# Performance work log

Measured on AMD Instinct MI355X. Metric: run time of the kernel, lower is better.

Reference implementation:

```python
import jax, jax.numpy as jnp
import numpy as np

C_IN, C_OUT, K, PAD, STRIDE = 128, 256, 3, 1, 1
H = W = 256


def setup_inputs() -> dict:
    key = jax.random.key(0)
    k1, k2, k3 = jax.random.split(key, 3)
    # batch=1: the original forward uses X_pad[0] for every batch index,
    # so with m=1 the buggy loop and a standard conv are mathematically identical.
    x = jax.random.normal(k1, (1, C_IN, H, W), dtype=jnp.float32)
    # nn.Parameter(torch.rand(...)) -> uniform[0,1)
    weight = jax.random.uniform(k2, (C_OUT, C_IN, K, K), dtype=jnp.float32)
    bias = jax.random.uniform(k3, (C_OUT,), dtype=jnp.float32)
    return {"x": x, "weight": weight, "bias": bias}


def reference(x, weight, bias):
    # Faithful math of convAppx.forward with FP_appx_mul treated as exact
    # multiply (FP_appx_mul is not defined in the source): a plain 2D
    # cross-correlation (no kernel flip, matching the sliced elementwise
    # product) with symmetric padding, stride 1, plus per-channel bias.
    z = jax.lax.conv_general_dilated(
        x, weight,
        window_strides=(STRIDE, STRIDE),
        padding=((PAD, PAD), (PAD, PAD)),
        dimension_numbers=("NCHW", "OIHW", "NCHW"),
    )
    return z + bias[None, :, None, None]
```

## Files before the change

kernel.cpp:

```cpp
#include <hip/hip_runtime.h>
#include <hip/hip_bf16.h>


typedef short bf16x8 __attribute__((ext_vector_type(8)));
typedef float f32x4 __attribute__((ext_vector_type(4)));
typedef unsigned short u16x4 __attribute__((ext_vector_type(4)));
typedef unsigned short u16x8 __attribute__((ext_vector_type(8)));

#define CIN   128
#define COUT  256
#define HH    256
#define WW    256
#define HP    258
#define ROWP  (HP * CIN)

static __device__ __forceinline__ unsigned short f2bf(float v) {
    __hip_bfloat16 b = __float2bfloat16(v);
    return *reinterpret_cast<unsigned short*>(&b);
}

static __device__ __forceinline__ void gload_lds16(const unsigned short* g, unsigned short* l) {
    __builtin_amdgcn_global_load_lds(
        (const __attribute__((address_space(1))) unsigned int*)g,
        (__attribute__((address_space(3))) unsigned int*)l, 16, 0, 0);
}

__global__ __launch_bounds__(256) void prep_kernel(const float* __restrict__ x,
                                                   const float* __restrict__ w,
                                                   unsigned short* __restrict__ xb,
                                                   unsigned short* __restrict__ wr) {
    int bid = blockIdx.x;
    int t   = threadIdx.x;

    if (bid < 65) {
        int i = bid * 256 + t;
        if (i < 16448) {
            u16x8 z = {0, 0, 0, 0, 0, 0, 0, 0};
            int off;
            if (i < 8256) {
                int r   = (i >= 4128) ? 1 : 0;
                int rem = i - r * 4128;
                off = (r * 257) * ROWP + rem * 8;
            } else {
                int j   = i - 8256;
                int col = j >> 12;
                int rem = j & 4095;
                int hp  = (rem >> 4) + 1;
                int c8  = rem & 15;
                off = hp * ROWP + (col * 257) * CIN + c8 * 8;
            }
            *(u16x8*)(&xb[off]) = z;
        }
    }

    if (bid < 128) {
        int p = bid * 256 + t;
        const float* src = w + p * 9;
        #pragma unroll
        for (int khw = 0; khw < 9; ++khw)
            wr[khw * (COUT * CIN) + p] = f2bf(src[khw]);
    }

    int h  = bid >> 2;
    int w0 = (bid & 3) * 64;
    __shared__ unsigned short tile[CIN * 72];

    int wq  = t & 15;
    int cib = t >> 4;
    for (int c0 = 0; c0 < CIN; c0 += 16) {
        int ci = c0 + cib;
        float4 v = *(const float4*)(x + ci * (HH * WW) + h * WW + w0 + wq * 4);
        u16x4 p;
        p.x = f2bf(v.x); p.y = f2bf(v.y); p.z = f2bf(v.z); p.w = f2bf(v.w);
        *(u16x4*)(&tile[ci * 72 + wq * 4]) = p;
    }
    __syncthreads();

    for (int it = 0; it < 4; ++it) {
        int idx = it * 256 + t;
        int ww_ = idx & 63;
        int c8  = idx >> 6;
        u16x8 o;
        #pragma unroll
        for (int j = 0; j < 8; ++j)
            o[j] = tile[(c8 * 8 + j) * 72 + ww_];
        int dst = ((h + 1) * HP + (w0 + ww_ + 1)) * CIN + c8 * 8;
        *(u16x8*)(&xb[dst]) = o;
    }
}

__global__ __launch_bounds__(512, 2) void conv_mfma_kernel(const unsigned short* __restrict__ xb,
                                                           const unsigned short* __restrict__ wr,
                                                           const float* __restrict__ bias,
                                                           float* __restrict__ out) {
    __shared__ unsigned short Bw[258 * 128];
    __shared__ unsigned short Ah[2][256 * 64];

    int bid = blockIdx.x;
    int h   = (bid & 7) * 32 + (bid >> 3);

    int t    = threadIdx.x;
    int lane = t & 63;
    int wave = t >> 6;
    int wm   = wave >> 1;
    int wn   = wave & 1;
    int quad = lane >> 4;
    int l16  = lane & 15;

    f32x4 acc[4][8];
    #pragma unroll
    for (int mi = 0; mi < 4; ++mi)
        #pragma unroll
        for (int ni = 0; ni < 8; ++ni)
            acc[mi][ni] = (f32x4){0.f, 0.f, 0.f, 0.f};

    auto stageA = [&](int idx, unsigned short* dst) {
        int khw_  = idx >> 1;
        int half_ = idx & 1;
        const unsigned short* wsrc = wr + (size_t)khw_ * (COUT * CIN) + half_ * 64;
        #pragma unroll
        for (int it = 0; it < 4; ++it) {
            int seg = it * 512 + t;
            int r   = seg >> 3;
            int s   = seg & 7;
            int c   = s ^ (r & 7);
            gload_lds16(wsrc + r * CIN + c * 8, &dst[seg * 8]);
        }
    };

    stageA(0, Ah[0]);

    for (int i = 0; i < 18; ++i) {
        int khw  = i >> 1;
        int half = i & 1;
        int kw   = khw % 3;

        if ((i % 6) == 0) {
            const unsigned short* xrow = xb + (size_t)(h + i / 6) * ROWP;
            #pragma unroll
            for (int it = 0; it < 8; ++it) {
                int seg = it * 512 + t;
                int col = seg >> 4;
                int s   = seg & 15;
                int c   = s ^ (col & 15);
                gload_lds16(xrow + col * CIN + c * 8, &Bw[seg * 8]);
            }
            if (t < 32) {
                int seg = 4096 + t;
                int col = seg >> 4;
                int s   = seg & 15;
                int c   = s ^ (col & 15);
                gload_lds16(xrow + col * CIN + c * 8, &Bw[seg * 8]);
            }
        }

        int nxt = (i + 1) % 18;
        stageA(nxt, Ah[nxt & 1]);

        asm volatile("s_waitcnt vmcnt(4)" ::: "memory");
        __builtin_amdgcn_s_barrier();
        __builtin_amdgcn_sched_barrier(0);

        const unsigned short* Acur = Ah[i & 1];
        __builtin_amdgcn_s_setprio(1);
        #pragma unroll
        for (int kkk = 0; kkk < 2; ++kkk) {
            int lc = kkk * 4 + quad;
            int cg = half * 8 + lc;
            bf16x8 af[4], bfr[8];
            #pragma unroll
            for (int mi = 0; mi < 4; ++mi) {
                int row = wm * 64 + mi * 16 + l16;
                af[mi] = *(bf16x8*)(&Acur[row * 64 + (lc ^ (l16 & 7)) * 8]);
            }
            #pragma unroll
            for (int ni = 0; ni < 8; ++ni) {
                int col = wn * 128 + ni * 16 + l16 + kw;
                bfr[ni] = *(bf16x8*)(&Bw[col * 128 + (cg ^ (col & 15)) * 8]);
            }
            #pragma unroll
            for (int mi = 0; mi < 4; ++mi)
                #pragma unroll
                for (int ni = 0; ni < 8; ++ni)
                    acc[mi][ni] = __builtin_amdgcn_mfma_f32_16x16x32_bf16(
                        af[mi], bfr[ni], acc[mi][ni], 0, 0, 0);
        }
        __builtin_amdgcn_s_setprio(0);

        asm volatile("s_waitcnt lgkmcnt(0)" ::: "memory");
        __builtin_amdgcn_s_barrier();
        __builtin_amdgcn_sched_barrier(0);
    }

    int sp0 = wn * 128 + l16;
    #pragma unroll
    for (int mi = 0; mi < 4; ++mi) {
        #pragma unroll
        for (int r = 0; r < 4; ++r) {
            int co = wm * 64 + mi * 16 + quad * 4 + r;
            float b = bias[co];
            float* orow = out + (size_t)co * (HH * WW) + h * WW + sp0;
            #pragma unroll
            for (int ni = 0; ni < 8; ++ni)
                orow[ni * 16] = acc[mi][ni][r] + b;
        }
    }
}

extern "C" void kernel_launch(void* const* d_in, const int* in_sizes, int n_in,
                              void* d_out, int out_size, void* d_ws, size_t ws_size,
                              hipStream_t stream) {
    const float* x    = (const float*)d_in[0];
    const float* w    = (const float*)d_in[1];
    const float* bias = (const float*)d_in[2];
    float* out        = (float*)d_out;

    unsigned short* xb = (unsigned short*)d_ws;
    unsigned short* wr = xb + (size_t)HP * HP * CIN;

    prep_kernel<<<dim3(1024), dim3(256), 0, stream>>>(x, w, xb, wr);
    conv_mfma_kernel<<<dim3(256), dim3(512), 0, stream>>>(xb, wr, bias, out);
}
```

Before: 136.2 us.

## Split input row into channel halves and interleave MFMA phases with barriers

The single full-channel input-row LDS buffer is replaced by two 64-channel half buffers, so the next input row can be prefetched one half at a time instead of reloading all 128 channels at once. The weight double buffer is now indexed by channel half. Each half-step is split into four phases: fragment reads, then an MFMA burst, with workgroup barriers around them. This ping-pong style schedule aims to overlap LDS reads with matrix math across waves and to hide global-to-LDS loads. The halo columns of the input tile are zeroed in LDS once rather than loaded. The cost is many more barriers per step and a full vmcnt(0) drain at the end of every half-step, which could stall the pipeline.

```diff
diff --git a/kernel.cpp b/kernel.cpp
--- a/kernel.cpp
+++ b/kernel.cpp
@@ -93,7 +93,7 @@
                                                            const unsigned short* __restrict__ wr,
                                                            const float* __restrict__ bias,
                                                            float* __restrict__ out) {
-    __shared__ unsigned short Bw[258 * 128];
+    __shared__ unsigned short Bh[2][258 * 64];
     __shared__ unsigned short Ah[2][256 * 64];
 
     int bid = blockIdx.x;
@@ -114,10 +114,9 @@
         for (int ni = 0; ni < 8; ++ni)
             acc[mi][ni] = (f32x4){0.f, 0.f, 0.f, 0.f};
 
-    auto stageA = [&](int idx, unsigned short* dst) {
-        int khw_  = idx >> 1;
-        int half_ = idx & 1;
+    auto stageA = [&](int khw_, int half_) {
         const unsigned short* wsrc = wr + (size_t)khw_ * (COUT * CIN) + half_ * 64;
+        unsigned short* dst = Ah[half_];
         #pragma unroll
         for (int it = 0; it < 4; ++it) {
             int seg = it * 512 + t;
@@ -127,69 +126,137 @@
             gload_lds16(wsrc + r * CIN + c * 8, &dst[seg * 8]);
         }
     };
-
-    stageA(0, Ah[0]);
-
-    for (int i = 0; i < 18; ++i) {
-        int khw  = i >> 1;
-        int half = i & 1;
-        int kw   = khw % 3;
-
-        if ((i % 6) == 0) {
-            const unsigned short* xrow = xb + (size_t)(h + i / 6) * ROWP;
+    auto stageB = [&](int kh_, int p) {
+        const unsigned short* xrow = xb + (size_t)(h + kh_) * ROWP + p * 64;
+        unsigned short* dst = Bh[p];
+        #pragma unroll
+        for (int it = 0; it < 4; ++it) {
+            int seg = it * 512 + t;
+            int col = (seg >> 3) + 1;
+            int s   = seg & 7;
+            int c   = s ^ (col & 7);
+            gload_lds16(xrow + col * CIN + c * 8, &dst[col * 64 + s * 8]);
+        }
+    };
+
+    if (t < 32) {
+        int buf = t >> 4, colsel = (t >> 3) & 1, s = t & 7;
+        int col = colsel ? 257 : 0;
+        u16x8 z = {0, 0, 0, 0, 0, 0, 0, 0};
+        *(u16x8*)(&Bh[buf][col * 64 + s * 8]) = z;
+    }
+    stageB(0, 0);
+    stageB(0, 1);
+    stageA(0, 0);
+    asm volatile("s_waitcnt vmcnt(0) lgkmcnt(0)" ::: "memory");
+    __builtin_amdgcn_s_barrier();
+    __builtin_amdgcn_sched_barrier(0);
+
+    #pragma unroll 1
+    for (int kh = 0; kh < 3; ++kh) {
+        #pragma unroll
+        for (int kw = 0; kw < 3; ++kw) {
+            int khw = kh * 3 + kw;
             #pragma unroll
-            for (int it = 0; it < 8; ++it) {
-                int seg = it * 512 + t;
-                int col = seg >> 4;
-                int s   = seg & 15;
-                int c   = s ^ (col & 15);
-                gload_lds16(xrow + col * CIN + c * 8, &Bw[seg * 8]);
+            for (int half = 0; half < 2; ++half) {
+                const unsigned short* Acur = Bh[0];
+                Acur = Ah[half];
+                const unsigned short* Bcur = Bh[half];
+                int a_sw = l16 & 7;
+
+                bf16x8 bfr[8], af0, af1, af2, af3;
+
+                {
+                    int lc = quad;
+                    #pragma unroll
+                    for (int ni = 0; ni < 8; ++ni) {
+                        int col = wn * 128 + ni * 16 + l16 + kw;
+                        bfr[ni] = *(bf16x8*)(&Bcur[col * 64 + (lc ^ (col & 7)) * 8]);
+                    }
+                    af0 = *(bf16x8*)(&Acur[(wm * 64 +  0 + l16) * 64 + (lc ^ a_sw) * 8]);
+                    af1 = *(bf16x8*)(&Acur[(wm * 64 + 16 + l16) * 64 + (lc ^ a_sw) * 8]);
+                }
+                if (half == 0) {
+                    if (kw == 0 && kh > 0) stageB(kh, 1);
+                    stageA(khw, 1);
+                } else {
+                    if (kw == 2 && kh < 2) stageB(kh + 1, 0);
+                    stageA((khw == 8) ? 0 : khw + 1, 0);
+                }
+                __builtin_amdgcn_s_barrier();
+                asm volatile("s_waitcnt lgkmcnt(0)" ::: "memory");
+                __builtin_amdgcn_sched_barrier(0);
+                __builtin_amdgcn_s_setprio(1);
+                #pragma unroll
+                for (int ni = 0; ni < 8; ++ni) {
+                    acc[0][ni] = __builtin_amdgcn_mfma_f32_16x16x32_bf16(af0, bfr[ni], acc[0][ni], 0, 0, 0);
+                    acc[1][ni] = __builtin_amdgcn_mfma_f32_16x16x32_bf16(af1, bfr[ni], acc[1][ni], 0, 0, 0);
+                }
+                __builtin_amdgcn_s_setprio(0);
+                __builtin_amdgcn_s_barrier();
+                __builtin_amdgcn_sched_barrier(0);
+
+                {
+                    int lc = quad;
+                    af2 = *(bf16x8*)(&Acur[(wm * 64 + 32 + l16) * 64 + (lc ^ a_sw) * 8]);
+                    af3 = *(bf16x8*)(&Acur[(wm * 64 + 48 + l16) * 64 + (lc ^ a_sw) * 8]);
+                }
+                __builtin_amdgcn_s_barrier();
+                asm volatile("s_waitcnt lgkmcnt(0)" ::: "memory");
+                __builtin_amdgcn_sched_barrier(0);
+                __builtin_amdgcn_s_setprio(1);
+                #pragma unroll
+                for (int ni = 0; ni < 8; ++ni) {
+                    acc[2][ni] = __builtin_amdgcn_mfma_f32_16x16x32_bf16(af2, bfr[ni], acc[2][ni], 0, 0, 0);
+                    acc[3][ni] = __builtin_amdgcn_mfma_f32_16x16x32_bf16(af3, bfr[ni], acc[3][ni], 0, 0, 0);
+                }
+                __builtin_amdgcn_s_setprio(0);
+                __builtin_amdgcn_s_barrier();
+                __builtin_amdgcn_sched_barrier(0);
+
+                {
+                    int lc = 4 + quad;
+                    #pragma unroll
+                    for (int ni = 0; ni < 8; ++ni) {
+                        int col = wn * 128 + ni * 16 + l16 + kw;
+                        bfr[ni] = *(bf16x8*)(&Bcur[col * 64 + (lc ^ (col & 7)) * 8]);
+                    }
+                    af0 = *(bf16x8*)(&Acur[(wm * 64 +  0 + l16) * 64 + (lc ^ a_sw) * 8]);
+                    af1 = *(bf16x8*)(&Acur[(wm * 64 + 16 + l16) * 64 + (lc ^ a_sw) * 8]);
+                }
+                __builtin_amdgcn_s_barrier();
+                asm volatile("s_waitcnt lgkmcnt(0)" ::: "memory");
+                __builtin_amdgcn_sched_barrier(0);
+                __builtin_amdgcn_s_setprio(1);
+                #pragma unroll
+                for (int ni = 0; ni < 8; ++ni) {
+                    acc[0][ni] = __builtin_amdgcn_mfma_f32_16x16x32_bf16(af0, bfr[ni], acc[0][ni], 0, 0, 0);
+                    acc[1][ni] = __builtin_amdgcn_mfma_f32_16x16x32_bf16(af1, bfr[ni], acc[1][ni], 0, 0, 0);
+                }
+                __builtin_amdgcn_s_setprio(0);
+                __builtin_amdgcn_s_barrier();
+                __builtin_amdgcn_sched_barrier(0);
+
+                {
+                    int lc = 4 + quad;
+                    af2 = *(bf16x8*)(&Acur[(wm * 64 + 32 + l16) * 64 + (lc ^ a_sw) * 8]);
+                    af3 = *(bf16x8*)(&Acur[(wm * 64 + 48 + l16) * 64 + (lc ^ a_sw) * 8]);
+                }
+                __builtin_amdgcn_s_barrier();
+                asm volatile("s_waitcnt lgkmcnt(0)" ::: "memory");
+                __builtin_amdgcn_sched_barrier(0);
+                __builtin_amdgcn_s_setprio(1);
+                #pragma unroll
+                for (int ni = 0; ni < 8; ++ni) {
+                    acc[2][ni] = __builtin_amdgcn_mfma_f32_16x16x32_bf16(af2, bfr[ni], acc[2][ni], 0, 0, 0);
+                    acc[3][ni] = __builtin_amdgcn_mfma_f32_16x16x32_bf16(af3, bfr[ni], acc[3][ni], 0, 0, 0);
+                }
+                __builtin_amdgcn_s_setprio(0);
+                asm volatile("s_waitcnt vmcnt(0)" ::: "memory");
+                __builtin_amdgcn_s_barrier();
+                __builtin_amdgcn_sched_barrier(0);
             }
-            if (t < 32) {
-                int seg = 4096 + t;
-                int col = seg >> 4;
-                int s   = seg & 15;
-                int c   = s ^ (col & 15);
-                gload_lds16(xrow + col * CIN + c * 8, &Bw[seg * 8]);
-            }
-        }
-
-        int nxt = (i + 1) % 18;
-        stageA(nxt, Ah[nxt & 1]);
-
-        asm volatile("s_waitcnt vmcnt(4)" ::: "memory");
-        __builtin_amdgcn_s_barrier();
-        __builtin_amdgcn_sched_barrier(0);
-
-        const unsigned short* Acur = Ah[i & 1];
-        __builtin_amdgcn_s_setprio(1);
-        #pragma unroll
-        for (int kkk = 0; kkk < 2; ++kkk) {
-            int lc = kkk * 4 + quad;
-            int cg = half * 8 + lc;
-            bf16x8 af[4], bfr[8];
-            #pragma unroll
-            for (int mi = 0; mi < 4; ++mi) {
-                int row = wm * 64 + mi * 16 + l16;
-                af[mi] = *(bf16x8*)(&Acur[row * 64 + (lc ^ (l16 & 7)) * 8]);
-            }
-            #pragma unroll
-            for (int ni = 0; ni < 8; ++ni) {
-                int col = wn * 128 + ni * 16 + l16 + kw;
-                bfr[ni] = *(bf16x8*)(&Bw[col * 128 + (cg ^ (col & 15)) * 8]);
-            }
-            #pragma unroll
-            for (int mi = 0; mi < 4; ++mi)
-                #pragma unroll
-                for (int ni = 0; ni < 8; ++ni)
-                    acc[mi][ni] = __builtin_amdgcn_mfma_f32_16x16x32_bf16(
-                        af[mi], bfr[ni], acc[mi][ni], 0, 0, 0);
-        }
-        __builtin_amdgcn_s_setprio(0);
-
-        asm volatile("s_waitcnt lgkmcnt(0)" ::: "memory");
-        __builtin_amdgcn_s_barrier();
-        __builtin_amdgcn_sched_barrier(0);
+        }
     }
 
     int sp0 = wn * 128 + l16;
```

Measured after the change: 148.8 us. 9.2% more time.

## Reuse B fragments across kw taps via DPP row rotation, drop A double-buffering

Applied to the files above, without the earlier changes.

Restructures the conv main loop into 6 iterations over (kh, cin-half). Each iteration stages the three kw weight slices at once, plus a half-channel input row. The kw-shifted B operands are built in registers from one LDS read using DPP row-rotate, which cuts LDS reads of the input row. The change also removes the overlapped double-buffered A prefetch and now waits for vmcnt(0) before every compute phase. That exposes global-load latency and adds DPP/select ALU work per MFMA group.

```diff
diff --git a/kernel.cpp b/kernel.cpp
--- a/kernel.cpp
+++ b/kernel.cpp
@@ -4,6 +4,7 @@
 
 typedef short bf16x8 __attribute__((ext_vector_type(8)));
 typedef float f32x4 __attribute__((ext_vector_type(4)));
+typedef int   i32x4 __attribute__((ext_vector_type(4)));
 typedef unsigned short u16x4 __attribute__((ext_vector_type(4)));
 typedef unsigned short u16x8 __attribute__((ext_vector_type(8)));
 
@@ -24,6 +25,18 @@
         (const __attribute__((address_space(1))) unsigned int*)g,
         (__attribute__((address_space(3))) unsigned int*)l, 16, 0, 0);
 }
+
+template<int CTRL>
+static __device__ __forceinline__ bf16x8 rotf(bf16x8 a) {
+    i32x4 ai = __builtin_bit_cast(i32x4, a);
+    i32x4 r;
+    #pragma unroll
+    for (int j = 0; j < 4; ++j)
+        r[j] = __builtin_amdgcn_mov_dpp(ai[j], CTRL, 0xF, 0xF, true);
+    return __builtin_bit_cast(bf16x8, r);
+}
+#define ROR_P1 0x12F
+#define ROR_P2 0x12E
 
 __global__ __launch_bounds__(256) void prep_kernel(const float* __restrict__ x,
                                                    const float* __restrict__ w,
@@ -93,8 +106,10 @@
                                                            const unsigned short* __restrict__ wr,
                                                            const float* __restrict__ bias,
                                                            float* __restrict__ out) {
-    __shared__ unsigned short Bw[258 * 128];
-    __shared__ unsigned short Ah[2][256 * 64];
+    __shared__ unsigned short A0[256 * 64];
+    __shared__ unsigned short A1[256 * 64];
+    __shared__ unsigned short A2[256 * 64];
+    __shared__ unsigned short Bs[258 * 64];
 
     int bid = blockIdx.x;
     int h   = (bid & 7) * 32 + (bid >> 3);
@@ -114,80 +129,94 @@
         for (int ni = 0; ni < 8; ++ni)
             acc[mi][ni] = (f32x4){0.f, 0.f, 0.f, 0.f};
 
-    auto stageA = [&](int idx, unsigned short* dst) {
-        int khw_  = idx >> 1;
-        int half_ = idx & 1;
-        const unsigned short* wsrc = wr + (size_t)khw_ * (COUT * CIN) + half_ * 64;
-        #pragma unroll
-        for (int it = 0; it < 4; ++it) {
-            int seg = it * 512 + t;
-            int r   = seg >> 3;
-            int s   = seg & 7;
-            int c   = s ^ (r & 7);
-            gload_lds16(wsrc + r * CIN + c * 8, &dst[seg * 8]);
-        }
-    };
-
-    stageA(0, Ah[0]);
-
-    for (int i = 0; i < 18; ++i) {
-        int khw  = i >> 1;
-        int half = i & 1;
-        int kw   = khw % 3;
-
-        if ((i % 6) == 0) {
-            const unsigned short* xrow = xb + (size_t)(h + i / 6) * ROWP;
-            #pragma unroll
-            for (int it = 0; it < 8; ++it) {
+    unsigned short* const Ap[3] = {A0, A1, A2};
+
+    #pragma unroll 1
+    for (int i = 0; i < 6; ++i) {
+        int kh     = i >> 1;
+        int cihalf = i & 1;
+
+        #pragma unroll
+        for (int p = 0; p < 3; ++p) {
+            const unsigned short* wsrc = wr + (size_t)(kh * 3 + p) * (COUT * CIN) + cihalf * 64;
+            unsigned short* dst = Ap[p];
+            #pragma unroll
+            for (int it = 0; it < 4; ++it) {
                 int seg = it * 512 + t;
-                int col = seg >> 4;
-                int s   = seg & 15;
-                int c   = s ^ (col & 15);
-                gload_lds16(xrow + col * CIN + c * 8, &Bw[seg * 8]);
-            }
-            if (t < 32) {
-                int seg = 4096 + t;
-                int col = seg >> 4;
-                int s   = seg & 15;
-                int c   = s ^ (col & 15);
-                gload_lds16(xrow + col * CIN + c * 8, &Bw[seg * 8]);
-            }
-        }
-
-        int nxt = (i + 1) % 18;
-        stageA(nxt, Ah[nxt & 1]);
-
-        asm volatile("s_waitcnt vmcnt(4)" ::: "memory");
+                int r   = seg >> 3;
+                int s   = seg & 7;
+                int c   = s ^ (r & 7);
+                gload_lds16(wsrc + r * CIN + c * 8, &dst[seg * 8]);
+            }
+        }
+        {
+            const unsigned short* xrow = xb + (size_t)(h + kh) * ROWP + cihalf * 64;
+            #pragma unroll
+            for (int it = 0; it < 4; ++it) {
+                int seg = it * 512 + t;
+                int col = seg >> 3;
+                int s   = seg & 7;
+                int c   = s ^ (col & 7);
+                gload_lds16(xrow + col * CIN + c * 8, &Bs[col * 64 + s * 8]);
+            }
+            if (t < 16) {
+                int seg = 2048 + t;
+                int col = seg >> 3;
+                int s   = seg & 7;
+                int c   = s ^ (col & 7);
+                gload_lds16(xrow + col * CIN + c * 8, &Bs[col * 64 + s * 8]);
+            }
+        }
+        asm volatile("s_waitcnt vmcnt(0)" ::: "memory");
         __builtin_amdgcn_s_barrier();
         __builtin_amdgcn_sched_barrier(0);
 
-        const unsigned short* Acur = Ah[i & 1];
-        __builtin_amdgcn_s_setprio(1);
-        #pragma unroll
-        for (int kkk = 0; kkk < 2; ++kkk) {
-            int lc = kkk * 4 + quad;
-            int cg = half * 8 + lc;
-            bf16x8 af[4], bfr[8];
+        #pragma unroll
+        for (int kk = 0; kk < 2; ++kk) {
+            int ck  = kk * 4 + quad;
+            int asl = (ck ^ (l16 & 7)) * 8;
+
+            bf16x8 af0[4], af1[4], af2[4];
             #pragma unroll
             for (int mi = 0; mi < 4; ++mi) {
-                int row = wm * 64 + mi * 16 + l16;
-                af[mi] = *(bf16x8*)(&Acur[row * 64 + (lc ^ (l16 & 7)) * 8]);
-            }
+                int ro = (wm * 64 + mi * 16 + l16) * 64;
+                af0[mi] = *(const bf16x8*)(&A0[ro + asl]);
+                af1[mi] = *(const bf16x8*)(&A1[ro + asl]);
+                af2[mi] = *(const bf16x8*)(&A2[ro + asl]);
+            }
+
+            auto rdB = [&](int ni_) -> bf16x8 {
+                int col = wn * 128 + ni_ * 16 + l16;
+                if (col > 257) col = 257;
+                return *(const bf16x8*)(&Bs[col * 64 + ((ck ^ (col & 7)) * 8)]);
+            };
+
+            bf16x8 cur = rdB(0);
             #pragma unroll
             for (int ni = 0; ni < 8; ++ni) {
-                int col = wn * 128 + ni * 16 + l16 + kw;
-                bfr[ni] = *(bf16x8*)(&Bw[col * 128 + (cg ^ (col & 15)) * 8]);
-            }
-            #pragma unroll
-            for (int mi = 0; mi < 4; ++mi)
+                bf16x8 nxt = rdB(ni + 1);
+                bf16x8 r1c = rotf<ROR_P1>(cur), r1n = rotf<ROR_P1>(nxt);
+                bf16x8 s1  = (l16 == 15) ? r1n : r1c;
+                bf16x8 r2c = rotf<ROR_P2>(cur), r2n = rotf<ROR_P2>(nxt);
+                bf16x8 s2  = (l16 >= 14) ? r2n : r2c;
+
+                __builtin_amdgcn_s_setprio(1);
                 #pragma unroll
-                for (int ni = 0; ni < 8; ++ni)
+                for (int mi = 0; mi < 4; ++mi)
                     acc[mi][ni] = __builtin_amdgcn_mfma_f32_16x16x32_bf16(
-                        af[mi], bfr[ni], acc[mi][ni], 0, 0, 0);
-        }
-        __builtin_amdgcn_s_setprio(0);
-
-        asm volatile("s_waitcnt lgkmcnt(0)" ::: "memory");
+                        af0[mi], cur, acc[mi][ni], 0, 0, 0);
+                #pragma unroll
+                for (int mi = 0; mi < 4; ++mi)
+                    acc[mi][ni] = __builtin_amdgcn_mfma_f32_16x16x32_bf16(
+                        af1[mi], s1, acc[mi][ni], 0, 0, 0);
+                #pragma unroll
+                for (int mi = 0; mi < 4; ++mi)
+                    acc[mi][ni] = __builtin_amdgcn_mfma_f32_16x16x32_bf16(
+                        af2[mi], s2, acc[mi][ni], 0, 0, 0);
+                __builtin_amdgcn_s_setprio(0);
+                cur = nxt;
+            }
+        }
         __builtin_amdgcn_s_barrier();
         __builtin_amdgcn_sched_barrier(0);
     }
```

Measured after the change: 136.9 us. Within noise of the previous version (+0.5%).
